# Optimization experiments

Hardware: AMD Instinct MI355X
Metric: run time of the kernel (lower is better)

The kernel has to match this reference:

```python
import jax, jax.numpy as jnp
import numpy as np


def _gru(x, h0, Wi, Wh, bi, bh):
    """PyTorch-equations GRU. x: (T,B,D), Wi: (3H,D), Wh: (3H,H). Returns (ys, hT)."""
    xW = jnp.einsum('tbd,gd->tbg', x, Wi) + bi  # (T,B,3H) precomputed input proj
    def step(h, xw):
        hw = h @ Wh.T + bh
        xr, xz, xn = jnp.split(xw, 3, axis=-1)
        hr, hz, hn = jnp.split(hw, 3, axis=-1)
        r = jax.nn.sigmoid(xr + hr)
        z = jax.nn.sigmoid(xz + hz)
        n = jnp.tanh(xn + r * hn)
        h_new = (1.0 - z) * n + z * h
        return h_new, h_new
    hT, ys = jax.lax.scan(step, h0, xW)
    return ys, hT


def _bigru(x, WiF, WhF, biF, bhF, WiB, WhB, biB, bhB):
    B = x.shape[1]
    H = WhF.shape[1]
    h0 = jnp.zeros((B, H), x.dtype)
    yf, hf = _gru(x, h0, WiF, WhF, biF, bhF)
    yb, hb = _gru(x[::-1], h0, WiB, WhB, biB, bhB)
    return jnp.concatenate([yf, yb[::-1]], axis=-1), jnp.stack([hf, hb], axis=0)


def _ln(x, g, b, eps=1e-5):
    mu = x.mean(-1, keepdims=True)
    var = ((x - mu) ** 2).mean(-1, keepdims=True)
    return (x - mu) * jax.lax.rsqrt(var + eps) * g + b


def _forward(tokens, emb,
             s_WiF, s_WhF, s_biF, s_bhF, s_lnF_g, s_lnF_b,
             s_Wi_f, s_Wh_f, s_bi_f, s_bh_f, s_Wi_b, s_Wh_b, s_bi_b, s_bh_b,
             s_ln_g, s_ln_b, s_linW, s_linb,
             d_WiF, d_WhF, d_biF, d_bhF, d_lnF_g, d_lnF_b,
             d_Wi_f, d_Wh_f, d_bi_f, d_bh_f, d_Wi_b, d_Wh_b, d_bi_b, d_bh_b,
             d_ln_g, d_ln_b, out_W, out_b):
    S, T, B = tokens.shape
    H = s_WhF.shape[1]
    # sentence loop is batch-independent -> fold sentences into batch
    x = emb[tokens]                                  # (S,T,B,E)
    x = x.transpose(1, 0, 2, 3).reshape(T, S * B, -1)  # (T, S*B, E)
    h0 = jnp.zeros((S * B, H), x.dtype)
    y, _ = _gru(x, h0, s_WiF, s_WhF, s_biF, s_bhF)
    y = _ln(y, s_lnF_g, s_lnF_b)
    y, _ = _bigru(y, s_Wi_f, s_Wh_f, s_bi_f, s_bh_f, s_Wi_b, s_Wh_b, s_bi_b, s_bh_b)
    y = _ln(y, s_ln_g, s_ln_b)
    y = jnp.tanh(y @ s_linW.T + s_linb)              # (T, S*B, H)
    store = y.mean(axis=0).reshape(S, B, H)          # per-sentence mean-pooled cell
    # document-level encoder over sentence sequence
    h0d = jnp.zeros((B, H), x.dtype)
    y, _ = _gru(store, h0d, d_WiF, d_WhF, d_biF, d_bhF)
    y = _ln(y, d_lnF_g, d_lnF_b)
    y, _ = _bigru(y, d_Wi_f, d_Wh_f, d_bi_f, d_bh_f, d_Wi_b, d_Wh_b, d_bi_b, d_bh_b)
    y = _ln(y, d_ln_g, d_ln_b)
    return jax.nn.sigmoid(y @ out_W.T + out_b)       # (S, B, O)


def setup_inputs() -> dict:
    V, E, H, O = 32000, 256, 256, 2
    S, T, B = 96, 32, 32
    keys = iter(jax.random.split(jax.random.key(0), 64))
    def g(shape, scale=0.06):
        return jax.random.normal(next(keys), shape, jnp.float32) * scale
    inp = {}
    inp['tokens'] = jax.random.randint(next(keys), (S, T, B), 0, V)
    inp['emb'] = g((V, E), 0.1)
    # sentence encoder: uni GRU (E->H), LN(H), bi GRU (H->H), LN(2H), linear 2H->H
    inp['s_WiF'] = g((3 * H, E)); inp['s_WhF'] = g((3 * H, H))
    inp['s_biF'] = jnp.zeros((3 * H,)); inp['s_bhF'] = jnp.zeros((3 * H,))
    inp['s_lnF_g'] = jnp.ones((H,)); inp['s_lnF_b'] = jnp.zeros((H,))
    inp['s_Wi_f'] = g((3 * H, H)); inp['s_Wh_f'] = g((3 * H, H))
    inp['s_bi_f'] = jnp.zeros((3 * H,)); inp['s_bh_f'] = jnp.zeros((3 * H,))
    inp['s_Wi_b'] = g((3 * H, H)); inp['s_Wh_b'] = g((3 * H, H))
    inp['s_bi_b'] = jnp.zeros((3 * H,)); inp['s_bh_b'] = jnp.zeros((3 * H,))
    inp['s_ln_g'] = jnp.ones((2 * H,)); inp['s_ln_b'] = jnp.zeros((2 * H,))
    inp['s_linW'] = g((H, 2 * H)); inp['s_linb'] = jnp.zeros((H,))
    # document encoder: uni GRU (H->H), LN(H), bi GRU (H->H), LN(2H)
    inp['d_WiF'] = g((3 * H, H)); inp['d_WhF'] = g((3 * H, H))
    inp['d_biF'] = jnp.zeros((3 * H,)); inp['d_bhF'] = jnp.zeros((3 * H,))
    inp['d_lnF_g'] = jnp.ones((H,)); inp['d_lnF_b'] = jnp.zeros((H,))
    inp['d_Wi_f'] = g((3 * H, H)); inp['d_Wh_f'] = g((3 * H, H))
    inp['d_bi_f'] = jnp.zeros((3 * H,)); inp['d_bh_f'] = jnp.zeros((3 * H,))
    inp['d_Wi_b'] = g((3 * H, H)); inp['d_Wh_b'] = g((3 * H, H))
    inp['d_bi_b'] = jnp.zeros((3 * H,)); inp['d_bh_b'] = jnp.zeros((3 * H,))
    inp['d_ln_g'] = jnp.ones((2 * H,)); inp['d_ln_b'] = jnp.zeros((2 * H,))
    inp['out_W'] = g((O, 2 * H)); inp['out_b'] = jnp.zeros((O,))
    return inp


def reference(tokens, emb,
              s_WiF, s_WhF, s_biF, s_bhF, s_lnF_g, s_lnF_b,
              s_Wi_f, s_Wh_f, s_bi_f, s_bh_f, s_Wi_b, s_Wh_b, s_bi_b, s_bh_b,
              s_ln_g, s_ln_b, s_linW, s_linb,
              d_WiF, d_WhF, d_biF, d_bhF, d_lnF_g, d_lnF_b,
              d_Wi_f, d_Wh_f, d_bi_f, d_bh_f, d_Wi_b, d_Wh_b, d_bi_b, d_bh_b,
              d_ln_g, d_ln_b, out_W, out_b):
    return _forward(tokens, emb,
                    s_WiF, s_WhF, s_biF, s_bhF, s_lnF_g, s_lnF_b,
                    s_Wi_f, s_Wh_f, s_bi_f, s_bh_f, s_Wi_b, s_Wh_b, s_bi_b, s_bh_b,
                    s_ln_g, s_ln_b, s_linW, s_linb,
                    d_WiF, d_WhF, d_biF, d_bhF, d_lnF_g, d_lnF_b,
                    d_Wi_f, d_Wh_f, d_bi_f, d_bh_f, d_Wi_b, d_Wh_b, d_bi_b, d_bh_b,
                    d_ln_g, d_ln_b, out_W, out_b)
```

## Files before the change

kernel.cpp:

```cpp
#include <hip/hip_runtime.h>


typedef __bf16 bf16;
typedef __bf16 bf16x8 __attribute__((ext_vector_type(8)));
typedef __bf16 bf16x4 __attribute__((ext_vector_type(4)));
typedef float  f32x4  __attribute__((ext_vector_type(4)));

static __device__ __forceinline__ f32x4 mfma16(bf16x8 a, bf16x8 b, f32x4 c) {
  return __builtin_amdgcn_mfma_f32_16x16x32_bf16(a, b, c, 0, 0, 0);
}
static __device__ __forceinline__ float sigm(float x) { return 1.f / (1.f + __expf(-x)); }
static __device__ __forceinline__ bf16x8 asbf(f32x4 v) {
  union { f32x4 f; bf16x8 b; } u; u.f = v; return u.b;
}
static __device__ __forceinline__ void wg_barrier() {
  asm volatile("s_waitcnt lgkmcnt(0)" ::: "memory");
  __builtin_amdgcn_s_barrier();
  __builtin_amdgcn_sched_barrier(0);
}

__global__ __launch_bounds__(256) void cvt_bf16(
    const float* __restrict__ s, bf16* __restrict__ d, int n4)
{
  int i = blockIdx.x * 256 + threadIdx.x;
  if (i < n4) {
    float4 v = ((const float4*)s)[i];
    bf16x4 o;
    o[0] = (bf16)v.x; o[1] = (bf16)v.y; o[2] = (bf16)v.z; o[3] = (bf16)v.w;
    ((bf16x4*)d)[i] = o;
  }
}

__global__ __launch_bounds__(256) void conv13(
    const float* s0, const float* s1, const float* s2, const float* s3,
    const float* s4, const float* s5, const float* s6, const float* s7,
    const float* s8, const float* s9, const float* s10, const float* s11,
    const float* s12, bf16* __restrict__ dst)
{
  const float* srcs[13] = {s0,s1,s2,s3,s4,s5,s6,s7,s8,s9,s10,s11,s12};
  int m = blockIdx.y;
  int n4 = (m == 12) ? 32768 : 49152;
  int i = blockIdx.x * 256 + threadIdx.x;
  if (i >= n4) return;
  float4 v = ((const float4*)srcs[m])[i];
  bf16x4 o;
  o[0] = (bf16)v.x; o[1] = (bf16)v.y; o[2] = (bf16)v.z; o[3] = (bf16)v.w;
  ((bf16x4*)(dst + (size_t)m * 196608))[i] = o;
}

__global__ __launch_bounds__(256) void xw_gemm(
    const bf16* __restrict__ X,
    const bf16* __restrict__ W0, const float* __restrict__ b0, bf16* __restrict__ o0,
    const bf16* __restrict__ W1, const float* __restrict__ b1, bf16* __restrict__ o1)
{
  const bf16* W = blockIdx.y ? W1 : W0;
  const float* bias = blockIdx.y ? b1 : b0;
  bf16* out = blockIdx.y ? o1 : o0;
  int wave = (int)blockIdx.x * 4 + (threadIdx.x >> 6);
  int g64 = wave / 48, ct = wave - g64 * 48;
  int lane = threadIdx.x & 63;
  int r16 = lane & 15, g4 = lane >> 4;
  const bf16* wp = W + (size_t)(ct * 16 + r16) * 256;
  const bf16* xb = X + ((size_t)g64 * 64 + r16) * 256;
  f32x4 a0 = {0,0,0,0}, a1 = {0,0,0,0}, a2 = {0,0,0,0}, a3 = {0,0,0,0};
#pragma unroll
  for (int kk = 0; kk < 8; kk++) {
    int k0 = kk * 32 + g4 * 8;
    bf16x8 wf = *(const bf16x8*)(wp + k0);
    a0 = mfma16(*(const bf16x8*)(xb + k0), wf, a0);
    a1 = mfma16(*(const bf16x8*)(xb + 4096 + k0), wf, a1);
    a2 = mfma16(*(const bf16x8*)(xb + 8192 + k0), wf, a2);
    a3 = mfma16(*(const bf16x8*)(xb + 12288 + k0), wf, a3);
  }
  float bv = bias[ct * 16 + r16];
#pragma unroll
  for (int rt = 0; rt < 4; rt++) {
    f32x4 ac = rt == 0 ? a0 : rt == 1 ? a1 : rt == 2 ? a2 : a3;
#pragma unroll
    for (int j = 0; j < 4; j++)
      out[(size_t)(g64 * 64 + rt * 16 + g4 * 4 + j) * 768 + ct * 16 + r16] = (bf16)(ac[j] + bv);
  }
}

__global__ __launch_bounds__(256) void xw_gather_gemm(
    const int* __restrict__ tok, const bf16* __restrict__ embb,
    const bf16* __restrict__ W, const float* __restrict__ bias,
    bf16* __restrict__ out, int c)
{
  int t = blockIdx.y;
  int wave = (int)blockIdx.x * 4 + (threadIdx.x >> 6);
  int g64 = wave / 48, ct = wave - g64 * 48;
  int lane = threadIdx.x & 63;
  int r16 = lane & 15, g4 = lane >> 4;
  const bf16* wp = W + (size_t)(ct * 16 + r16) * 256;
  const bf16* ap[4];
#pragma unroll
  for (int rt = 0; rt < 4; rt++) {
    int n = g64 * 64 + rt * 16 + r16;
    int tk = tok[((n >> 5) << 10) + (t << 5) + (n & 31)];
    ap[rt] = embb + (size_t)tk * 256;
  }
  f32x4 a0 = {0,0,0,0}, a1 = {0,0,0,0}, a2 = {0,0,0,0}, a3 = {0,0,0,0};
#pragma unroll
  for (int kk = 0; kk < 8; kk++) {
    int k0 = kk * 32 + g4 * 8;
    bf16x8 wf = *(const bf16x8*)(wp + k0);
    a0 = mfma16(*(const bf16x8*)(ap[0] + k0), wf, a0);
    a1 = mfma16(*(const bf16x8*)(ap[1] + k0), wf, a1);
    a2 = mfma16(*(const bf16x8*)(ap[2] + k0), wf, a2);
    a3 = mfma16(*(const bf16x8*)(ap[3] + k0), wf, a3);
  }
  float bv = bias[ct * 16 + r16];
#pragma unroll
  for (int rt = 0; rt < 4; rt++) {
    f32x4 ac = rt == 0 ? a0 : rt == 1 ? a1 : rt == 2 ? a2 : a3;
#pragma unroll
    for (int j = 0; j < 4; j++)
      out[((size_t)t * c + g64 * 64 + rt * 16 + g4 * 4 + j) * 768 + ct * 16 + r16] = (bf16)(ac[j] + bv);
  }
}

__global__ __launch_bounds__(512)
__attribute__((amdgpu_waves_per_eu(1, 2)))
void pgru(
    const bf16* __restrict__ xw0, const bf16* __restrict__ Wh0, const float* __restrict__ bh0,
    const bf16* __restrict__ xw1, const bf16* __restrict__ Wh1, const float* __restrict__ bh1,
    bf16* __restrict__ yout0, bf16* __restrict__ yout1, int ostride,
    const float* __restrict__ lng, const float* __restrict__ lnb,
    int steps, int Mtot, int rev0, int rev1)
{
  int dir = blockIdx.y;
  const bf16*  xw = dir ? xw1 : xw0;
  const bf16*  Wh = dir ? Wh1 : Wh0;
  const float* bh = dir ? bh1 : bh0;
  bf16* yout = dir ? yout1 : yout0;
  int rev = dir ? rev1 : rev0;

  __shared__ __align__(16) bf16 hbuf[16][264];
  __shared__ __align__(16) bf16 xbuf[2][16][776];

  int tid = threadIdx.x;
  int w = tid >> 6, lane = tid & 63, r16 = lane & 15, g4 = lane >> 4;
  int rowbase = (int)blockIdx.x * 16;
  int c0 = w * 32 + r16, c1 = w * 32 + 16 + r16;

  for (int i2 = tid; i2 < 528; i2 += 512) ((bf16x8*)hbuf)[i2] = (bf16x8){};

  f32x4 wr0[8], wz0[8], wn0[8], wr1[8], wz1[8], wn1[8];
  {
    const bf16* W0 = Wh + (size_t)c0 * 256;
    const bf16* W1 = Wh + (size_t)c1 * 256;
#pragma unroll
    for (int kk = 0; kk < 8; kk++) {
      int k0 = kk * 32 + g4 * 8;
      wr0[kk] = *(const f32x4*)(W0 + k0);          asm volatile("" : "+v"(wr0[kk]));
      wz0[kk] = *(const f32x4*)(W0 + 65536 + k0);  asm volatile("" : "+v"(wz0[kk]));
      wn0[kk] = *(const f32x4*)(W0 + 131072 + k0); asm volatile("" : "+v"(wn0[kk]));
      wr1[kk] = *(const f32x4*)(W1 + k0);          asm volatile("" : "+v"(wr1[kk]));
      wz1[kk] = *(const f32x4*)(W1 + 65536 + k0);  asm volatile("" : "+v"(wz1[kk]));
      wn1[kk] = *(const f32x4*)(W1 + 131072 + k0); asm volatile("" : "+v"(wn1[kk]));
    }
  }
  float bhr0 = bh[c0], bhz0 = bh[c0 + 256], bhn0 = bh[c0 + 512];
  float bhr1 = bh[c1], bhz1 = bh[c1 + 256], bhn1 = bh[c1 + 512];

  {
    int st0 = rev ? steps - 1 : 0;
    const bf16* src = xw + ((size_t)st0 * Mtot + rowbase) * 768;
#pragma unroll
    for (int it = 0; it < 3; it++) {
      int idx = it * 4096 + tid * 8;
      f32x4 v = *(const f32x4*)(src + idx);
      int m = idx / 768, k = idx - m * 768;
      *(f32x4*)&xbuf[0][m][k] = v;
    }
  }
  wg_barrier();

  for (int i = 0; i < steps; i++) {
    int cur = i & 1;
    int st = rev ? steps - 1 - i : i;
    f32x4 pf0 = {}, pf1 = {}, pf2 = {};
    bool havepf = (i + 1 < steps);
    if (havepf) {
      int stn = rev ? steps - 2 - i : i + 1;
      const bf16* src = xw + ((size_t)stn * Mtot + rowbase) * 768;
      pf0 = *(const f32x4*)(src + tid * 8);
      pf1 = *(const f32x4*)(src + 4096 + tid * 8);
      pf2 = *(const f32x4*)(src + 8192 + tid * 8);
    }
    f32x4 ar0 = {0,0,0,0}, az0 = {0,0,0,0}, an0 = {0,0,0,0};
    f32x4 ar1 = {0,0,0,0}, az1 = {0,0,0,0}, an1 = {0,0,0,0};
#pragma unroll
    for (int kk = 0; kk < 8; kk++) {
      bf16x8 a = *(const bf16x8*)&hbuf[r16][kk * 32 + g4 * 8];
      ar0 = mfma16(a, asbf(wr0[kk]), ar0);
      az0 = mfma16(a, asbf(wz0[kk]), az0);
      an0 = mfma16(a, asbf(wn0[kk]), an0);
      ar1 = mfma16(a, asbf(wr1[kk]), ar1);
      az1 = mfma16(a, asbf(wz1[kk]), az1);
      an1 = mfma16(a, asbf(wn1[kk]), an1);
    }
    float hn0[4], hn1[4];
#pragma unroll
    for (int j = 0; j < 4; j++) {
      int m = g4 * 4 + j;
      const bf16* xq = &xbuf[cur][m][0];
      {
        float r = sigm((float)xq[c0] + ar0[j] + bhr0);
        float z = sigm((float)xq[c0 + 256] + az0[j] + bhz0);
        float n = tanhf((float)xq[c0 + 512] + r * (an0[j] + bhn0));
        hn0[j] = (1.f - z) * n + z * (float)hbuf[m][c0];
      }
      {
        float r = sigm((float)xq[c1] + ar1[j] + bhr1);
        float z = sigm((float)xq[c1 + 256] + az1[j] + bhz1);
        float n = tanhf((float)xq[c1 + 512] + r * (an1[j] + bhn1));
        hn1[j] = (1.f - z) * n + z * (float)hbuf[m][c1];
      }
    }
    wg_barrier();
#pragma unroll
    for (int j = 0; j < 4; j++) {
      int m = g4 * 4 + j;
      hbuf[m][c0] = (bf16)hn0[j];
      hbuf[m][c1] = (bf16)hn1[j];
    }
    if (havepf) {
      { int idx = tid * 8;        int m = idx / 768, k = idx - m * 768; *(f32x4*)&xbuf[cur ^ 1][m][k] = pf0; }
      { int idx = 4096 + tid * 8; int m = idx / 768, k = idx - m * 768; *(f32x4*)&xbuf[cur ^ 1][m][k] = pf1; }
      { int idx = 8192 + tid * 8; int m = idx / 768, k = idx - m * 768; *(f32x4*)&xbuf[cur ^ 1][m][k] = pf2; }
    }
    if (!lng) {
#pragma unroll
      for (int j = 0; j < 4; j++) {
        size_t ro = ((size_t)st * Mtot + rowbase + g4 * 4 + j) * ostride;
        yout[ro + c0] = (bf16)hn0[j];
        yout[ro + c1] = (bf16)hn1[j];
      }
    }
    wg_barrier();
    if (lng) {
#pragma unroll
      for (int rr = 0; rr < 2; rr++) {
        int r = w * 2 + rr;
        bf16x4 v4 = *(const bf16x4*)&hbuf[r][lane * 4];
        float v[4]; float sm = 0.f, sq = 0.f;
#pragma unroll
        for (int j = 0; j < 4; j++) { v[j] = (float)v4[j]; sm += v[j]; sq += v[j] * v[j]; }
        for (int msk = 32; msk; msk >>= 1) { sm += __shfl_xor(sm, msk); sq += __shfl_xor(sq, msk); }
        float mu  = sm * (1.f / 256.f);
        float var = sq * (1.f / 256.f) - mu * mu;
        float inv = rsqrtf(fmaxf(var, 0.f) + 1e-5f);
        bf16x4 o;
#pragma unroll
        for (int j = 0; j < 4; j++)
          o[j] = (bf16)((v[j] - mu) * inv * lng[lane * 4 + j] + lnb[lane * 4 + j]);
        *(bf16x4*)&yout[((size_t)st * Mtot + rowbase + r) * ostride + lane * 4] = o;
      }
    }
  }
}

__global__ __launch_bounds__(256) void sent_tail_part(
    const bf16* __restrict__ hf, const bf16* __restrict__ hb,
    const float* __restrict__ gam, const float* __restrict__ bet,
    const bf16* __restrict__ W, const float* __restrict__ bias,
    float* __restrict__ part, int c)
{
  int wave = threadIdx.x >> 6;
  int lane = threadIdx.x & 63;
  int r16 = lane & 15, g4 = lane >> 4;
  int r0 = (int)blockIdx.x << 4;
  int tg = blockIdx.y;
  size_t rowoff = (size_t)(r0 + r16) * 256;

  f32x4 ms0 = {0,0,0,0}, ms1 = {0,0,0,0}, ms2 = {0,0,0,0}, ms3 = {0,0,0,0};

  for (int tt = 0; tt < 4; tt++) {
    int t = tg * 4 + tt;
    const bf16* pf = hf + (size_t)t * c * 256 + rowoff;
    const bf16* pb = hb + (size_t)t * c * 256 + rowoff;
    bf16x8 xv[16];
    float s = 0.f, sq = 0.f;
#pragma unroll
    for (int kk = 0; kk < 16; kk++) {
      int k0 = kk * 32 + g4 * 8;
      xv[kk] = (kk < 8) ? *(const bf16x8*)(pf + k0) : *(const bf16x8*)(pb + k0 - 256);
#pragma unroll
      for (int j = 0; j < 8; j++) { float f = (float)xv[kk][j]; s += f; sq += f * f; }
    }
    s  += __shfl_xor(s, 16);  s  += __shfl_xor(s, 32);
    sq += __shfl_xor(sq, 16); sq += __shfl_xor(sq, 32);
    float mu  = s * (1.f / 512.f);
    float var = sq * (1.f / 512.f) - mu * mu;
    float inv = rsqrtf(fmaxf(var, 0.f) + 1e-5f);
#pragma unroll
    for (int kk = 0; kk < 16; kk++) {
      int k0 = kk * 32 + g4 * 8;
      float ga[8], be[8];
      *(float4*)(ga)     = *(const float4*)(gam + k0);
      *(float4*)(ga + 4) = *(const float4*)(gam + k0 + 4);
      *(float4*)(be)     = *(const float4*)(bet + k0);
      *(float4*)(be + 4) = *(const float4*)(bet + k0 + 4);
#pragma unroll
      for (int j = 0; j < 8; j++)
        xv[kk][j] = (bf16)(((float)xv[kk][j] - mu) * inv * ga[j] + be[j]);
    }
#pragma unroll
    for (int tc = 0; tc < 4; tc++) {
      int cj = wave * 64 + tc * 16;
      const bf16* wp = W + (size_t)(cj + r16) * 512;
      f32x4 acc = {0,0,0,0};
#pragma unroll
      for (int kk = 0; kk < 16; kk++)
        acc = mfma16(xv[kk], *(const bf16x8*)(wp + kk * 32 + g4 * 8), acc);
      float bb = bias[cj + r16];
      f32x4* msp = (tc == 0) ? &ms0 : (tc == 1) ? &ms1 : (tc == 2) ? &ms2 : &ms3;
#pragma unroll
      for (int j = 0; j < 4; j++) (*msp)[j] += tanhf(acc[j] + bb);
    }
  }
#pragma unroll
  for (int tc = 0; tc < 4; tc++) {
    int cj = wave * 64 + tc * 16;
    f32x4 ms = (tc == 0) ? ms0 : (tc == 1) ? ms1 : (tc == 2) ? ms2 : ms3;
#pragma unroll
    for (int j = 0; j < 4; j++)
      part[((size_t)tg * c + r0 + g4 * 4 + j) * 256 + cj + r16] = ms[j];
  }
}

__global__ __launch_bounds__(256) void tail_reduce(
    const float* __restrict__ part, bf16* __restrict__ out, int c)
{
  int idx = blockIdx.x * 256 + threadIdx.x;
  float s = 0.f;
#pragma unroll
  for (int g = 0; g < 8; g++) s += part[(size_t)g * c * 256 + idx];
  out[idx] = (bf16)(s * 0.03125f);
}

__global__ __launch_bounds__(256) void ln_out_head(
    const bf16* __restrict__ X, const float* __restrict__ lng, const float* __restrict__ lnb,
    const float* __restrict__ W, const float* __restrict__ bias, float* __restrict__ out)
{
  int w = threadIdx.x >> 6, lane = threadIdx.x & 63;
  int row = (int)blockIdx.x * 4 + w;
  bf16x8 v8 = *(const bf16x8*)&X[(size_t)row * 512 + lane * 8];
  float v[8]; float sm = 0.f, sq = 0.f;
#pragma unroll
  for (int j = 0; j < 8; j++) { v[j] = (float)v8[j]; sm += v[j]; sq += v[j] * v[j]; }
  for (int msk = 32; msk; msk >>= 1) { sm += __shfl_xor(sm, msk); sq += __shfl_xor(sq, msk); }
  float mu  = sm * (1.f / 512.f);
  float var = sq * (1.f / 512.f) - mu * mu;
  float inv = rsqrtf(fmaxf(var, 0.f) + 1e-5f);
  float a0 = 0.f, a1 = 0.f;
  int base = lane * 8;
#pragma unroll
  for (int j = 0; j < 8; j++) {
    float y = (v[j] - mu) * inv * lng[base + j] + lnb[base + j];
    a0 += y * W[base + j];
    a1 += y * W[512 + base + j];
  }
  for (int msk = 32; msk; msk >>= 1) { a0 += __shfl_xor(a0, msk); a1 += __shfl_xor(a1, msk); }
  if (lane == 0) {
    out[(size_t)row * 2 + 0] = sigm(a0 + bias[0]);
    out[(size_t)row * 2 + 1] = sigm(a1 + bias[1]);
  }
}

extern "C" void kernel_launch(void* const* d_in, const int* in_sizes, int n_in,
                              void* d_out, int out_size, void* d_ws, size_t ws_size,
                              hipStream_t stream)
{
  (void)in_sizes; (void)n_in; (void)out_size;
  const int*   tokens = (const int*)d_in[0];
  const float* emb    = (const float*)d_in[1];
  auto fp = [&](int i) { return (const float*)d_in[i]; };
  const float *s_WiF = fp(2),  *s_WhF = fp(3),  *s_biF = fp(4),  *s_bhF = fp(5);
  const float *s_lnF_g = fp(6), *s_lnF_b = fp(7);
  const float *s_Wi_f = fp(8),  *s_Wh_f = fp(9),  *s_bi_f = fp(10), *s_bh_f = fp(11);
  const float *s_Wi_b = fp(12), *s_Wh_b = fp(13), *s_bi_b = fp(14), *s_bh_b = fp(15);
  const float *s_ln_g = fp(16), *s_ln_b = fp(17), *s_linW = fp(18), *s_linb = fp(19);
  const float *dWiF = fp(20), *dWhF = fp(21), *dbiF = fp(22), *dbhF = fp(23);
  const float *d_lnF_g = fp(24), *d_lnF_b = fp(25);
  const float *dWi_f = fp(26), *dWh_f = fp(27), *dbi_f = fp(28), *dbh_f = fp(29);
  const float *dWi_b = fp(30), *dWh_b = fp(31), *dbi_b = fp(32), *dbh_b = fp(33);
  const float *d_ln_g = fp(34), *d_ln_b = fp(35), *out_W = fp(36), *out_b = fp(37);

  const int T = 32, S = 96;
  const int GW = 196608;

  bf16* wc = (bf16*)d_ws;
  bf16 *c_sWiF = wc,         *c_sWhF = wc + GW;
  bf16 *c_sWif = wc + 2*GW,  *c_sWhf = wc + 3*GW;
  bf16 *c_sWib = wc + 4*GW,  *c_sWhb = wc + 5*GW;
  bf16 *c_dWiF = wc + 6*GW,  *c_dWhF = wc + 7*GW;
  bf16 *c_dWif = wc + 8*GW,  *c_dWhf = wc + 9*GW;
  bf16 *c_dWib = wc + 10*GW, *c_dWhb = wc + 11*GW;
  bf16 *c_linW = wc + 12*GW;
  const size_t WB = (size_t)(12 * GW + 131072) * 2;
  bf16* embb = (bf16*)((char*)d_ws + WB);
  const size_t EB = (size_t)32000 * 256 * 2;

  conv13<<<dim3(192, 13), 256, 0, stream>>>(
      s_WiF, s_WhF, s_Wi_f, s_Wh_f, s_Wi_b, s_Wh_b,
      dWiF, dWhF, dWi_f, dWh_f, dWi_b, dWh_b, s_linW, wc);
  cvt_bf16<<<8000, 256, 0, stream>>>(emb, embb, 2048000);

  char* ws = (char*)d_ws + WB + EB;
  bf16* store = (bf16*)ws;
  bf16* yd1ln = store + (size_t)3072 * 256;
  bf16* ybid  = yd1ln + (size_t)3072 * 256;
  bf16* xw_u  = ybid  + (size_t)3072 * 512;
  bf16* xwdf  = xw_u  + (size_t)3072 * 768;
  bf16* xwdb  = xwdf  + (size_t)3072 * 768;
  const size_t fixedB = WB + EB
      + ((size_t)3072 * 256 * 2 + (size_t)3072 * 512 + (size_t)3 * 3072 * 768) * 2;

  int c = 3072;
  while (c > 192 && fixedB + (size_t)98304 * c > ws_size) c >>= 1;
  char* cb = (char*)d_ws + fixedB;
  bf16*  xw   = (bf16*)cb;
  bf16*  y1ln = (bf16*)(cb + (size_t)49152 * c);
  bf16*  hf   = (bf16*)(cb + (size_t)65536 * c);
  bf16*  hb   = (bf16*)(cb + (size_t)81920 * c);
  float* part = (float*)cb;

  for (int base = 0; base < 3072; base += c) {
    const int* tkb = tokens + (size_t)base * 32;
    xw_gather_gemm<<<dim3((c / 64) * 12, T), 256, 0, stream>>>(
        tkb, embb, c_sWiF, s_biF, xw, c);
    pgru<<<dim3(c / 16, 1), 512, 0, stream>>>(
        xw, c_sWhF, s_bhF, nullptr, nullptr, nullptr,
        y1ln, nullptr, 256, s_lnF_g, s_lnF_b, T, c, 0, 0);
    xw_gemm<<<dim3((T * c / 64) * 12, 1), 256, 0, stream>>>(
        y1ln, c_sWif, s_bi_f, xw, nullptr, nullptr, nullptr);
    pgru<<<dim3(c / 16, 1), 512, 0, stream>>>(
        xw, c_sWhf, s_bh_f, nullptr, nullptr, nullptr,
        hf, nullptr, 256, nullptr, nullptr, T, c, 0, 0);
    xw_gemm<<<dim3((T * c / 64) * 12, 1), 256, 0, stream>>>(
        y1ln, c_sWib, s_bi_b, xw, nullptr, nullptr, nullptr);
    pgru<<<dim3(c / 16, 1), 512, 0, stream>>>(
        xw, c_sWhb, s_bh_b, nullptr, nullptr, nullptr,
        hb, nullptr, 256, nullptr, nullptr, T, c, 1, 0);
    sent_tail_part<<<dim3(c / 16, 8), 256, 0, stream>>>(
        hf, hb, s_ln_g, s_ln_b, c_linW, s_linb, part, c);
    tail_reduce<<<c, 256, 0, stream>>>(part, store + (size_t)base * 256, c);
  }

  xw_gemm<<<dim3((3072 / 64) * 12, 1), 256, 0, stream>>>(
      store, c_dWiF, dbiF, xw_u, nullptr, nullptr, nullptr);
  pgru<<<dim3(2, 1), 512, 0, stream>>>(
      xw_u, c_dWhF, dbhF, nullptr, nullptr, nullptr,
      yd1ln, nullptr, 256, d_lnF_g, d_lnF_b, S, 32, 0, 0);
  xw_gemm<<<dim3((3072 / 64) * 12, 2), 256, 0, stream>>>(
      yd1ln, c_dWif, dbi_f, xwdf, c_dWib, dbi_b, xwdb);
  pgru<<<dim3(2, 2), 512, 0, stream>>>(
      xwdf, c_dWhf, dbh_f, xwdb, c_dWhb, dbh_b,
      ybid, ybid + 256, 512, nullptr, nullptr, S, 32, 0, 1);
  ln_out_head<<<768, 256, 0, stream>>>(ybid, d_ln_g, d_ln_b, out_W, out_b,
                                       (float*)d_out);
}
```

Measured before the change: 3.870 ms.

## Stage GRU input projections via direct global-to-LDS loads and fold biases

```diff
diff --git a/kernel.cpp b/kernel.cpp
--- a/kernel.cpp
+++ b/kernel.cpp
@@ -17,6 +17,11 @@
   asm volatile("s_waitcnt lgkmcnt(0)" ::: "memory");
   __builtin_amdgcn_s_barrier();
   __builtin_amdgcn_sched_barrier(0);
+}
+static __device__ __forceinline__ void gload16(const bf16* g, bf16* l) {
+  __builtin_amdgcn_global_load_lds(
+      (const __attribute__((address_space(1))) void*)g,
+      (__attribute__((address_space(3))) void*)l, 16, 0, 0);
 }
 
 __global__ __launch_bounds__(256) void cvt_bf16(
@@ -46,6 +51,20 @@
   bf16x4 o;
   o[0] = (bf16)v.x; o[1] = (bf16)v.y; o[2] = (bf16)v.z; o[3] = (bf16)v.w;
   ((bf16x4*)(dst + (size_t)m * 196608))[i] = o;
+}
+
+__global__ __launch_bounds__(256) void prep_bias(
+    const float* b0i, const float* b0h, const float* b1i, const float* b1h,
+    const float* b2i, const float* b2h, const float* b3i, const float* b3h,
+    const float* b4i, const float* b4h, const float* b5i, const float* b5h,
+    float* __restrict__ out)
+{
+  const float* bis[6] = {b0i,b1i,b2i,b3i,b4i,b5i};
+  const float* bhs[6] = {b0h,b1h,b2h,b3h,b4h,b5h};
+  int g = blockIdx.y;
+  int i = blockIdx.x * 256 + threadIdx.x;
+  if (i < 768)
+    out[g * 768 + i] = bis[g][i] + (i < 512 ? bhs[g][i] : 0.f);
 }
 
 __global__ __launch_bounds__(256) void xw_gemm(
@@ -137,12 +156,14 @@
   int rev = dir ? rev1 : rev0;
 
   __shared__ __align__(16) bf16 hbuf[16][264];
-  __shared__ __align__(16) bf16 xbuf[2][16][776];
+  __shared__ __align__(16) bf16 xbuf[2][8][3][16][32];
+  __shared__ bf16 ldspad[12544];
 
   int tid = threadIdx.x;
   int w = tid >> 6, lane = tid & 63, r16 = lane & 15, g4 = lane >> 4;
   int rowbase = (int)blockIdx.x * 16;
-  int c0 = w * 32 + r16, c1 = w * 32 + 16 + r16;
+  int c0 = w * 32 + r16, c1 = c0 + 16;
+  if (steps == 0) ldspad[tid] = (bf16)0.f;
 
   for (int i2 = tid; i2 < 528; i2 += 512) ((bf16x8*)hbuf)[i2] = (bf16x8){};
 
@@ -161,61 +182,63 @@
       wn1[kk] = *(const f32x4*)(W1 + 131072 + k0); asm volatile("" : "+v"(wn1[kk]));
     }
   }
-  float bhr0 = bh[c0], bhz0 = bh[c0 + 256], bhn0 = bh[c0 + 512];
-  float bhr1 = bh[c1], bhz1 = bh[c1 + 256], bhn1 = bh[c1 + 512];
-
-  {
-    int st0 = rev ? steps - 1 : 0;
-    const bf16* src = xw + ((size_t)st0 * Mtot + rowbase) * 768;
-#pragma unroll
-    for (int it = 0; it < 3; it++) {
-      int idx = it * 4096 + tid * 8;
-      f32x4 v = *(const f32x4*)(src + idx);
-      int m = idx / 768, k = idx - m * 768;
-      *(f32x4*)&xbuf[0][m][k] = v;
-    }
-  }
+  float bhn0 = bh[c0 + 512], bhn1 = bh[c1 + 512];
+
+  auto stage = [&](int b, int st) {
+    int row = rowbase + (lane >> 2);
+    const bf16* s = xw + ((size_t)st * Mtot + row) * 768 + w * 32 + (lane & 3) * 8;
+    gload16(s,       &xbuf[b][w][0][0][0]);
+    gload16(s + 256, &xbuf[b][w][1][0][0]);
+    gload16(s + 512, &xbuf[b][w][2][0][0]);
+  };
+  stage(0, rev ? steps - 1 : 0);
   wg_barrier();
 
   for (int i = 0; i < steps; i++) {
     int cur = i & 1;
     int st = rev ? steps - 1 - i : i;
-    f32x4 pf0 = {}, pf1 = {}, pf2 = {};
-    bool havepf = (i + 1 < steps);
-    if (havepf) {
-      int stn = rev ? steps - 2 - i : i + 1;
-      const bf16* src = xw + ((size_t)stn * Mtot + rowbase) * 768;
-      pf0 = *(const f32x4*)(src + tid * 8);
-      pf1 = *(const f32x4*)(src + 4096 + tid * 8);
-      pf2 = *(const f32x4*)(src + 8192 + tid * 8);
-    }
-    f32x4 ar0 = {0,0,0,0}, az0 = {0,0,0,0}, an0 = {0,0,0,0};
-    f32x4 ar1 = {0,0,0,0}, az1 = {0,0,0,0}, an1 = {0,0,0,0};
-#pragma unroll
-    for (int kk = 0; kk < 8; kk++) {
-      bf16x8 a = *(const bf16x8*)&hbuf[r16][kk * 32 + g4 * 8];
-      ar0 = mfma16(a, asbf(wr0[kk]), ar0);
-      az0 = mfma16(a, asbf(wz0[kk]), az0);
-      an0 = mfma16(a, asbf(wn0[kk]), an0);
-      ar1 = mfma16(a, asbf(wr1[kk]), ar1);
-      az1 = mfma16(a, asbf(wz1[kk]), az1);
-      an1 = mfma16(a, asbf(wn1[kk]), an1);
-    }
+    if (i + 1 < steps) {
+      stage(cur ^ 1, rev ? steps - 2 - i : i + 1);
+      asm volatile("s_waitcnt vmcnt(3)" ::: "memory");
+    } else {
+      asm volatile("s_waitcnt vmcnt(0)" ::: "memory");
+    }
+    __builtin_amdgcn_sched_barrier(0);
+
     float hn0[4], hn1[4];
-#pragma unroll
-    for (int j = 0; j < 4; j++) {
-      int m = g4 * 4 + j;
-      const bf16* xq = &xbuf[cur][m][0];
-      {
-        float r = sigm((float)xq[c0] + ar0[j] + bhr0);
-        float z = sigm((float)xq[c0 + 256] + az0[j] + bhz0);
-        float n = tanhf((float)xq[c0 + 512] + r * (an0[j] + bhn0));
+    {
+      f32x4 a0 = {0,0,0,0}, a1 = {0,0,0,0}, a2 = {0,0,0,0};
+#pragma unroll
+      for (int kk = 0; kk < 8; kk++) {
+        bf16x8 a = *(const bf16x8*)&hbuf[r16][kk * 32 + g4 * 8];
+        a0 = mfma16(a, asbf(wr0[kk]), a0);
+        a1 = mfma16(a, asbf(wz0[kk]), a1);
+        a2 = mfma16(a, asbf(wn0[kk]), a2);
+      }
+#pragma unroll
+      for (int j = 0; j < 4; j++) {
+        int m = g4 * 4 + j;
+        float r = sigm((float)xbuf[cur][w][0][m][r16] + a0[j]);
+        float z = sigm((float)xbuf[cur][w][1][m][r16] + a1[j]);
+        float n = tanhf((float)xbuf[cur][w][2][m][r16] + r * (a2[j] + bhn0));
         hn0[j] = (1.f - z) * n + z * (float)hbuf[m][c0];
       }
-      {
-        float r = sigm((float)xq[c1] + ar1[j] + bhr1);
-        float z = sigm((float)xq[c1 + 256] + az1[j] + bhz1);
-        float n = tanhf((float)xq[c1 + 512] + r * (an1[j] + bhn1));
+    }
+    {
+      f32x4 a0 = {0,0,0,0}, a1 = {0,0,0,0}, a2 = {0,0,0,0};
+#pragma unroll
+      for (int kk = 0; kk < 8; kk++) {
+        bf16x8 a = *(const bf16x8*)&hbuf[r16][kk * 32 + g4 * 8];
+        a0 = mfma16(a, asbf(wr1[kk]), a0);
+        a1 = mfma16(a, asbf(wz1[kk]), a1);
+        a2 = mfma16(a, asbf(wn1[kk]), a2);
+      }
+#pragma unroll
+      for (int j = 0; j < 4; j++) {
+        int m = g4 * 4 + j;
+        float r = sigm((float)xbuf[cur][w][0][m][r16 + 16] + a0[j]);
+        float z = sigm((float)xbuf[cur][w][1][m][r16 + 16] + a1[j]);
+        float n = tanhf((float)xbuf[cur][w][2][m][r16 + 16] + r * (a2[j] + bhn1));
         hn1[j] = (1.f - z) * n + z * (float)hbuf[m][c1];
       }
     }
@@ -225,11 +248,6 @@
       int m = g4 * 4 + j;
       hbuf[m][c0] = (bf16)hn0[j];
       hbuf[m][c1] = (bf16)hn1[j];
-    }
-    if (havepf) {
-      { int idx = tid * 8;        int m = idx / 768, k = idx - m * 768; *(f32x4*)&xbuf[cur ^ 1][m][k] = pf0; }
-      { int idx = 4096 + tid * 8; int m = idx / 768, k = idx - m * 768; *(f32x4*)&xbuf[cur ^ 1][m][k] = pf1; }
-      { int idx = 8192 + tid * 8; int m = idx / 768, k = idx - m * 768; *(f32x4*)&xbuf[cur ^ 1][m][k] = pf2; }
     }
     if (!lng) {
 #pragma unroll
@@ -403,20 +421,27 @@
   const size_t WB = (size_t)(12 * GW + 131072) * 2;
   bf16* embb = (bf16*)((char*)d_ws + WB);
   const size_t EB = (size_t)32000 * 256 * 2;
+  float* bmod = (float*)((char*)d_ws + WB + EB);
+  const size_t BMB = 6 * 768 * 4;
 
   conv13<<<dim3(192, 13), 256, 0, stream>>>(
       s_WiF, s_WhF, s_Wi_f, s_Wh_f, s_Wi_b, s_Wh_b,
       dWiF, dWhF, dWi_f, dWh_f, dWi_b, dWh_b, s_linW, wc);
   cvt_bf16<<<8000, 256, 0, stream>>>(emb, embb, 2048000);
-
-  char* ws = (char*)d_ws + WB + EB;
+  prep_bias<<<dim3(3, 6), 256, 0, stream>>>(
+      s_biF, s_bhF, s_bi_f, s_bh_f, s_bi_b, s_bh_b,
+      dbiF, dbhF, dbi_f, dbh_f, dbi_b, dbh_b, bmod);
+  const float *bm_sF = bmod, *bm_sf = bmod + 768, *bm_sb = bmod + 1536;
+  const float *bm_dF = bmod + 2304, *bm_df = bmod + 3072, *bm_db = bmod + 3840;
+
+  char* ws = (char*)d_ws + WB + EB + BMB;
   bf16* store = (bf16*)ws;
   bf16* yd1ln = store + (size_t)3072 * 256;
   bf16* ybid  = yd1ln + (size_t)3072 * 256;
   bf16* xw_u  = ybid  + (size_t)3072 * 512;
   bf16* xwdf  = xw_u  + (size_t)3072 * 768;
   bf16* xwdb  = xwdf  + (size_t)3072 * 768;
-  const size_t fixedB = WB + EB
+  const size_t fixedB = WB + EB + BMB
       + ((size_t)3072 * 256 * 2 + (size_t)3072 * 512 + (size_t)3 * 3072 * 768) * 2;
 
   int c = 3072;
@@ -431,17 +456,17 @@
   for (int base = 0; base < 3072; base += c) {
     const int* tkb = tokens + (size_t)base * 32;
     xw_gather_gemm<<<dim3((c / 64) * 12, T), 256, 0, stream>>>(
-        tkb, embb, c_sWiF, s_biF, xw, c);
+        tkb, embb, c_sWiF, bm_sF, xw, c);
     pgru<<<dim3(c / 16, 1), 512, 0, stream>>>(
         xw, c_sWhF, s_bhF, nullptr, nullptr, nullptr,
         y1ln, nullptr, 256, s_lnF_g, s_lnF_b, T, c, 0, 0);
     xw_gemm<<<dim3((T * c / 64) * 12, 1), 256, 0, stream>>>(
-        y1ln, c_sWif, s_bi_f, xw, nullptr, nullptr, nullptr);
+        y1ln, c_sWif, bm_sf, xw, nullptr, nullptr, nullptr);
     pgru<<<dim3(c / 16, 1), 512, 0, stream>>>(
         xw, c_sWhf, s_bh_f, nullptr, nullptr, nullptr,
         hf, nullptr, 256, nullptr, nullptr, T, c, 0, 0);
     xw_gemm<<<dim3((T * c / 64) * 12, 1), 256, 0, stream>>>(
-        y1ln, c_sWib, s_bi_b, xw, nullptr, nullptr, nullptr);
+        y1ln, c_sWib, bm_sb, xw, nullptr, nullptr, nullptr);
     pgru<<<dim3(c / 16, 1), 512, 0, stream>>>(
         xw, c_sWhb, s_bh_b, nullptr, nullptr, nullptr,
         hb, nullptr, 256, nullptr, nullptr, T, c, 1, 0);
@@ -451,12 +476,12 @@
   }
 
   xw_gemm<<<dim3((3072 / 64) * 12, 1), 256, 0, stream>>>(
-      store, c_dWiF, dbiF, xw_u, nullptr, nullptr, nullptr);
+      store, c_dWiF, bm_dF, xw_u, nullptr, nullptr, nullptr);
   pgru<<<dim3(2, 1), 512, 0, stream>>>(
       xw_u, c_dWhF, dbhF, nullptr, nullptr, nullptr,
       yd1ln, nullptr, 256, d_lnF_g, d_lnF_b, S, 32, 0, 0);
   xw_gemm<<<dim3((3072 / 64) * 12, 2), 256, 0, stream>>>(
-      yd1ln, c_dWif, dbi_f, xwdf, c_dWib, dbi_b, xwdb);
+      yd1ln, c_dWif, bm_df, xwdf, c_dWib, bm_db, xwdb);
   pgru<<<dim3(2, 2), 512, 0, stream>>>(
       xwdf, c_dWhf, dbh_f, xwdb, c_dWhb, dbh_b,
       ybid, ybid + 256, 512, nullptr, nullptr, S, 32, 0, 1);
```

After: 3.635 ms. -6.1%, faster.
